# Performance work log

Hardware: AMD Instinct MI355X
Metric: run time of the kernel (lower is better)

Reference implementation:

```python
import jax, jax.numpy as jnp
import numpy as np
from jax import lax

BN_EPS = 1e-3  # Keras BatchNormalization default


def ste_sign(x):
    # larq ste_sign forward: +1 for x >= 0, -1 otherwise
    return jnp.where(x >= 0, 1.0, -1.0).astype(x.dtype)


def conv2d_valid(x, w):
    # x: NHWC, w: HWIO, stride 1, VALID padding
    return lax.conv_general_dilated(
        x, w, window_strides=(1, 1), padding='VALID',
        dimension_numbers=('NHWC', 'HWIO', 'NHWC'))


def maxpool2(x):
    return lax.reduce_window(x, -jnp.inf, lax.max,
                             (1, 2, 2, 1), (1, 2, 2, 1), 'VALID')


def bn_infer(x, mean, var, beta):
    # BatchNormalization(scale=False): center only
    return (x - mean) * lax.rsqrt(var + BN_EPS) + beta


def setup_inputs() -> dict:
    key = jax.random.key(0)
    ks = jax.random.split(key, 16)
    B, H, W, C = 256, 64, 64, 3
    inp = {
        'inputs': jax.random.normal(ks[0], (B, H, W, C), jnp.float32),
        'w1': jax.random.normal(ks[1], (3, 3, 3, 32), jnp.float32) * 0.1,
        'w2': jax.random.normal(ks[2], (3, 3, 32, 64), jnp.float32) * 0.1,
        'w3': jax.random.normal(ks[3], (3, 3, 64, 64), jnp.float32) * 0.1,
        'd1w': jax.random.normal(ks[4], (12 * 12 * 64, 64), jnp.float32) * 0.05,
        'd2w': jax.random.normal(ks[5], (64, 10), jnp.float32) * 0.1,
    }
    for i, (name, c) in enumerate([('bn1', 32), ('bn2', 64), ('bn3', 64), ('bn4', 64), ('bn5', 10)]):
        kk = jax.random.split(ks[6 + i], 3)
        inp[name + '_mean'] = jax.random.normal(kk[0], (c,), jnp.float32) * 0.1
        inp[name + '_var'] = jax.random.uniform(kk[1], (c,), jnp.float32, 0.5, 1.5)
        inp[name + '_beta'] = jax.random.normal(kk[2], (c,), jnp.float32) * 0.1
    return inp


def reference(inputs, w1, w2, w3, d1w, d2w,
              bn1_mean, bn1_var, bn1_beta,
              bn2_mean, bn2_var, bn2_beta,
              bn3_mean, bn3_var, bn3_beta,
              bn4_mean, bn4_var, bn4_beta,
              bn5_mean, bn5_var, bn5_beta):
    # conv1: kernel quantized only (no input quantizer)
    x = conv2d_valid(inputs, ste_sign(w1))           # [B,62,62,32]
    x = maxpool2(x)                                   # [B,31,31,32]
    x = bn_infer(x, bn1_mean, bn1_var, bn1_beta)
    # conv2: input + kernel quantized
    x = conv2d_valid(ste_sign(x), ste_sign(w2))       # [B,29,29,64]
    x = maxpool2(x)                                   # [B,14,14,64]
    x = bn_infer(x, bn2_mean, bn2_var, bn2_beta)
    x = conv2d_valid(ste_sign(x), ste_sign(w3))       # [B,12,12,64]
    x = bn_infer(x, bn3_mean, bn3_var, bn3_beta)
    x = x.reshape(x.shape[0], -1)                     # [B,9216]
    x = ste_sign(x) @ ste_sign(d1w)                   # [B,64]
    x = bn_infer(x, bn4_mean, bn4_var, bn4_beta)
    x = ste_sign(x) @ ste_sign(d2w)                   # [B,10]
    x = bn_infer(x, bn5_mean, bn5_var, bn5_beta)
    return jax.nn.softmax(x, axis=-1)
```

## Files before the change

### kernel.cpp

```cpp
#include <hip/hip_runtime.h>

typedef unsigned int u32;
typedef unsigned long long u64;

#define BN_EPS 1e-3f

static const size_t OFF_BITS1 = 0;
static const size_t OFF_BITS2 = 984064;
static const size_t OFF_BITS3 = 1385472;
static const size_t OFF_BITSD = 1680384;
static const size_t OFF_W2B   = 1682432;
static const size_t OFF_W3B   = 1684736;
static const size_t OFF_D1WB  = 1689344;
static const size_t OFF_D2WB  = 1763072;
static const size_t OFF_T1    = 1763200;
static const size_t OFF_T2    = 1763328;
static const size_t OFF_T3    = 1763584;
static const size_t OFF_T4    = 1763840;

__global__ __launch_bounds__(256) void k_prep(
    const float* __restrict__ w2, const float* __restrict__ w3,
    const float* __restrict__ d1w, const float* __restrict__ d2w,
    const float* __restrict__ m1, const float* __restrict__ v1, const float* __restrict__ be1,
    const float* __restrict__ m2, const float* __restrict__ v2, const float* __restrict__ be2,
    const float* __restrict__ m3, const float* __restrict__ v3, const float* __restrict__ be3,
    const float* __restrict__ m4, const float* __restrict__ v4, const float* __restrict__ be4,
    u32* __restrict__ w2b, u64* __restrict__ w3b, u64* __restrict__ d1wb,
    u64* __restrict__ d2wb, float* __restrict__ t1, float* __restrict__ t2,
    float* __restrict__ t3, float* __restrict__ t4)
{
    int blk = blockIdx.x, tid = threadIdx.x;
    if (blk < 36) {
        int idx = blk * 256 + tid;
        int wi = idx >> 6, oc = idx & 63;
        u64 bits = 0;
        for (int j = 0; j < 64; ++j)
            bits |= (u64)(d1w[(wi * 64 + j) * 64 + oc] >= 0.f) << j;
        d1wb[idx] = bits;
    } else if (blk < 39) {
        int idx = (blk - 36) * 256 + tid;
        if (idx < 576) {
            int tap = idx >> 6, oc = idx & 63;
            u32 bits = 0;
            for (int ic = 0; ic < 32; ++ic)
                bits |= (u32)(w2[(tap * 32 + ic) * 64 + oc] >= 0.f) << ic;
            w2b[idx] = bits;
        }
    } else if (blk < 42) {
        int idx = (blk - 39) * 256 + tid;
        if (idx < 576) {
            int tap = idx >> 6, oc = idx & 63;
            u64 bits = 0;
            for (int ic = 0; ic < 64; ++ic)
                bits |= (u64)(w3[(tap * 64 + ic) * 64 + oc] >= 0.f) << ic;
            w3b[idx] = bits;
        }
    } else {
        if (tid < 32)       t1[tid]      = m1[tid] - be1[tid] * sqrtf(v1[tid] + BN_EPS);
        else if (tid < 96)  { int c = tid - 32;  t2[c] = m2[c] - be2[c] * sqrtf(v2[c] + BN_EPS); }
        else if (tid < 160) { int c = tid - 96;  t3[c] = m3[c] - be3[c] * sqrtf(v3[c] + BN_EPS); }
        else if (tid < 224) { int c = tid - 160; t4[c] = m4[c] - be4[c] * sqrtf(v4[c] + BN_EPS); }
        else if (tid < 234) {
            int oc = tid - 224;
            u64 bits = 0;
            for (int j = 0; j < 64; ++j)
                bits |= (u64)(d2w[j * 10 + oc] >= 0.f) << j;
            d2wb[oc] = bits;
        }
    }
}

__global__ __launch_bounds__(256) void k_conv1(
    const float* __restrict__ inp, const float* __restrict__ w1,
    const float* __restrict__ t1, u32* __restrict__ bits1)
{
    __shared__ float wf[32 * 28];
    __shared__ float t1s[32];
    int tid = threadIdx.x;
    for (int i = tid; i < 864; i += 256) {
        int oc = i / 27, tap = i - oc * 27;
        wf[oc * 28 + tap] = (w1[tap * 32 + oc] >= 0.f) ? 1.f : -1.f;
    }
    if (tid < 32) t1s[tid] = t1[tid];
    __syncthreads();

    int gid = blockIdx.x * 256 + tid;
    int b = gid / 961;
    int p = gid - b * 961;
    int ph = p / 31, pw = p - ph * 31;

    float x[4][4][3];
    const float* base = inp + ((b * 64 + 2 * ph) * 64 + 2 * pw) * 3;
#pragma unroll
    for (int i = 0; i < 4; ++i)
#pragma unroll
        for (int j = 0; j < 4; ++j)
#pragma unroll
            for (int k = 0; k < 3; ++k)
                x[i][j][k] = base[(i * 64 + j) * 3 + k];

    u32 word = 0;
#pragma unroll 1
    for (int oc = 0; oc < 32; ++oc) {
        float wv[28];
        const float4* wq = reinterpret_cast<const float4*>(wf + oc * 28);
#pragma unroll
        for (int q = 0; q < 7; ++q) {
            float4 t = wq[q];
            wv[4 * q] = t.x; wv[4 * q + 1] = t.y; wv[4 * q + 2] = t.z; wv[4 * q + 3] = t.w;
        }
        float s00 = 0.f, s01 = 0.f, s10 = 0.f, s11 = 0.f;
#pragma unroll
        for (int ky = 0; ky < 3; ++ky)
#pragma unroll
            for (int kx = 0; kx < 3; ++kx)
#pragma unroll
                for (int ic = 0; ic < 3; ++ic) {
                    float w = wv[(ky * 3 + kx) * 3 + ic];
                    s00 = fmaf(w, x[ky][kx][ic], s00);
                    s01 = fmaf(w, x[ky][kx + 1][ic], s01);
                    s10 = fmaf(w, x[ky + 1][kx][ic], s10);
                    s11 = fmaf(w, x[ky + 1][kx + 1][ic], s11);
                }
        float m = fmaxf(fmaxf(s00, s01), fmaxf(s10, s11));
        if (m >= t1s[oc]) word |= (1u << oc);
    }
    bits1[gid] = word;
}

__global__ __launch_bounds__(256) void k_conv2(
    const u32* __restrict__ bits1, const u32* __restrict__ w2b,
    const float* __restrict__ t2, u64* __restrict__ bits2)
{
    int lane = threadIdx.x & 63;
    int wid = blockIdx.x * 4 + (threadIdx.x >> 6);
    int b = wid / 196;
    int p = wid - b * 196;
    int ph = p / 14, pw = p - ph * 14;

    const u32* xb = bits1 + b * 961 + (2 * ph) * 31 + 2 * pw;
    u32 xw[4][4];
#pragma unroll
    for (int i = 0; i < 4; ++i)
#pragma unroll
        for (int j = 0; j < 4; ++j)
            xw[i][j] = xb[i * 31 + j];

    u32 wv[9];
#pragma unroll
    for (int t = 0; t < 9; ++t) wv[t] = w2b[t * 64 + lane];

    int mn = 1 << 30;
#pragma unroll
    for (int dy = 0; dy < 2; ++dy)
#pragma unroll
        for (int dx = 0; dx < 2; ++dx) {
            int s = 0;
#pragma unroll
            for (int ky = 0; ky < 3; ++ky)
#pragma unroll
                for (int kx = 0; kx < 3; ++kx)
                    s += __popc(xw[dy + ky][dx + kx] ^ wv[ky * 3 + kx]);
            mn = min(mn, s);
        }
    float val = (float)(288 - 2 * mn);
    u64 word = __ballot(val >= t2[lane]);
    if (lane == 0) bits2[wid] = word;
}

__global__ __launch_bounds__(256) void k_conv3(
    const u64* __restrict__ bits2, const u64* __restrict__ w3b,
    const float* __restrict__ t3, u64* __restrict__ bits3)
{
    int lane = threadIdx.x & 63;
    int wid = blockIdx.x * 4 + (threadIdx.x >> 6);
    int b = wid / 144;
    int p = wid - b * 144;
    int h = p / 12, w = p - h * 12;

    const u64* xb = bits2 + b * 196 + h * 14 + w;
    u64 xw[9];
#pragma unroll
    for (int ky = 0; ky < 3; ++ky)
#pragma unroll
        for (int kx = 0; kx < 3; ++kx)
            xw[ky * 3 + kx] = xb[ky * 14 + kx];

    int s = 0;
#pragma unroll
    for (int t = 0; t < 9; ++t)
        s += __popcll(xw[t] ^ w3b[t * 64 + lane]);
    float val = (float)(576 - 2 * s);
    u64 word = __ballot(val >= t3[lane]);
    if (lane == 0) bits3[wid] = word;
}

__global__ __launch_bounds__(256) void k_dense1(
    const u64* __restrict__ bits3, const u64* __restrict__ d1wb,
    const float* __restrict__ t4, u64* __restrict__ bitsD)
{
    int lane = threadIdx.x & 63;
    int b = blockIdx.x * 4 + (threadIdx.x >> 6);
    const u64* xb = bits3 + b * 144;
    int s = 0;
#pragma unroll 8
    for (int w = 0; w < 144; ++w)
        s += __popcll(xb[w] ^ d1wb[w * 64 + lane]);
    float val = (float)(9216 - 2 * s);
    u64 word = __ballot(val >= t4[lane]);
    if (lane == 0) bitsD[b] = word;
}

__global__ __launch_bounds__(256) void k_dense2(
    const u64* __restrict__ bitsD, const u64* __restrict__ d2wb,
    const float* __restrict__ m5, const float* __restrict__ v5,
    const float* __restrict__ be5, float* __restrict__ out)
{
    int b = threadIdx.x;
    u64 xv = bitsD[b];
    float y[10];
    float mx = -1e30f;
#pragma unroll
    for (int j = 0; j < 10; ++j) {
        int v = 64 - 2 * (int)__popcll(xv ^ d2wb[j]);
        y[j] = ((float)v - m5[j]) * rsqrtf(v5[j] + BN_EPS) + be5[j];
        mx = fmaxf(mx, y[j]);
    }
    float sum = 0.f;
#pragma unroll
    for (int j = 0; j < 10; ++j) { y[j] = expf(y[j] - mx); sum += y[j]; }
    float inv = 1.f / sum;
#pragma unroll
    for (int j = 0; j < 10; ++j) out[b * 10 + j] = y[j] * inv;
}

extern "C" void kernel_launch(void* const* d_in, const int* in_sizes, int n_in,
                              void* d_out, int out_size, void* d_ws, size_t ws_size,
                              hipStream_t stream)
{
    const float* inp = (const float*)d_in[0];
    const float* w1  = (const float*)d_in[1];
    const float* w2  = (const float*)d_in[2];
    const float* w3  = (const float*)d_in[3];
    const float* d1w = (const float*)d_in[4];
    const float* d2w = (const float*)d_in[5];
    const float* m1 = (const float*)d_in[6],  *v1 = (const float*)d_in[7],  *be1 = (const float*)d_in[8];
    const float* m2 = (const float*)d_in[9],  *v2 = (const float*)d_in[10], *be2 = (const float*)d_in[11];
    const float* m3 = (const float*)d_in[12], *v3 = (const float*)d_in[13], *be3 = (const float*)d_in[14];
    const float* m4 = (const float*)d_in[15], *v4 = (const float*)d_in[16], *be4 = (const float*)d_in[17];
    const float* m5 = (const float*)d_in[18], *v5 = (const float*)d_in[19], *be5 = (const float*)d_in[20];

    char* ws = (char*)d_ws;
    u32* bits1 = (u32*)(ws + OFF_BITS1);
    u64* bits2 = (u64*)(ws + OFF_BITS2);
    u64* bits3 = (u64*)(ws + OFF_BITS3);
    u64* bitsD = (u64*)(ws + OFF_BITSD);
    u32* w2b   = (u32*)(ws + OFF_W2B);
    u64* w3b   = (u64*)(ws + OFF_W3B);
    u64* d1wb  = (u64*)(ws + OFF_D1WB);
    u64* d2wb  = (u64*)(ws + OFF_D2WB);
    float* t1  = (float*)(ws + OFF_T1);
    float* t2  = (float*)(ws + OFF_T2);
    float* t3  = (float*)(ws + OFF_T3);
    float* t4  = (float*)(ws + OFF_T4);

    k_prep  <<<43,    256, 0, stream>>>(w2, w3, d1w, d2w,
                                        m1, v1, be1, m2, v2, be2,
                                        m3, v3, be3, m4, v4, be4,
                                        w2b, w3b, d1wb, d2wb, t1, t2, t3, t4);
    k_conv1 <<<961,   256, 0, stream>>>(inp, w1, t1, bits1);
    k_conv2 <<<12544, 256, 0, stream>>>(bits1, w2b, t2, bits2);
    k_conv3 <<<9216,  256, 0, stream>>>(bits2, w3b, t3, bits3);
    k_dense1<<<64,    256, 0, stream>>>(bits3, d1wb, t4, bitsD);
    k_dense2<<<1,     256, 0, stream>>>(bitsD, d2wb, m5, v5, be5, (float*)d_out);
}
```

Baseline: 168.7 us.

## Fuse weight prep into conv1 and conv3+dense1+dense2 into one per-batch kernel

Merges the weight-binarization prep kernel into the conv1 launch as extra blocks, with conv1 computing its own BN threshold inline. Conv3, dense1 and dense2 are fused into one kernel with one block per batch sample. Conv3 output bits stay in shared memory, dense1 is split across four wavefronts with a shared-memory reduction, and softmax uses 16-lane shuffles. This cuts launches from six to three and removes the bits3/bitsD global round trips, but the tail runs only 256 blocks, which may limit parallelism.

```diff
diff --git a/kernel.cpp b/kernel.cpp
--- a/kernel.cpp
+++ b/kernel.cpp
@@ -7,81 +7,78 @@
 
 static const size_t OFF_BITS1 = 0;
 static const size_t OFF_BITS2 = 984064;
-static const size_t OFF_BITS3 = 1385472;
-static const size_t OFF_BITSD = 1680384;
 static const size_t OFF_W2B   = 1682432;
 static const size_t OFF_W3B   = 1684736;
 static const size_t OFF_D1WB  = 1689344;
 static const size_t OFF_D2WB  = 1763072;
-static const size_t OFF_T1    = 1763200;
 static const size_t OFF_T2    = 1763328;
 static const size_t OFF_T3    = 1763584;
 static const size_t OFF_T4    = 1763840;
 
-__global__ __launch_bounds__(256) void k_prep(
+__global__ __launch_bounds__(256) void k_head(
+    const float* __restrict__ inp, const float* __restrict__ w1,
+    const float* __restrict__ m1, const float* __restrict__ v1, const float* __restrict__ be1,
     const float* __restrict__ w2, const float* __restrict__ w3,
     const float* __restrict__ d1w, const float* __restrict__ d2w,
-    const float* __restrict__ m1, const float* __restrict__ v1, const float* __restrict__ be1,
     const float* __restrict__ m2, const float* __restrict__ v2, const float* __restrict__ be2,
     const float* __restrict__ m3, const float* __restrict__ v3, const float* __restrict__ be3,
     const float* __restrict__ m4, const float* __restrict__ v4, const float* __restrict__ be4,
+    u32* __restrict__ bits1,
     u32* __restrict__ w2b, u64* __restrict__ w3b, u64* __restrict__ d1wb,
-    u64* __restrict__ d2wb, float* __restrict__ t1, float* __restrict__ t2,
-    float* __restrict__ t3, float* __restrict__ t4)
-{
-    int blk = blockIdx.x, tid = threadIdx.x;
-    if (blk < 36) {
-        int idx = blk * 256 + tid;
-        int wi = idx >> 6, oc = idx & 63;
-        u64 bits = 0;
-        for (int j = 0; j < 64; ++j)
-            bits |= (u64)(d1w[(wi * 64 + j) * 64 + oc] >= 0.f) << j;
-        d1wb[idx] = bits;
-    } else if (blk < 39) {
-        int idx = (blk - 36) * 256 + tid;
-        if (idx < 576) {
-            int tap = idx >> 6, oc = idx & 63;
-            u32 bits = 0;
-            for (int ic = 0; ic < 32; ++ic)
-                bits |= (u32)(w2[(tap * 32 + ic) * 64 + oc] >= 0.f) << ic;
-            w2b[idx] = bits;
-        }
-    } else if (blk < 42) {
-        int idx = (blk - 39) * 256 + tid;
-        if (idx < 576) {
-            int tap = idx >> 6, oc = idx & 63;
-            u64 bits = 0;
-            for (int ic = 0; ic < 64; ++ic)
-                bits |= (u64)(w3[(tap * 64 + ic) * 64 + oc] >= 0.f) << ic;
-            w3b[idx] = bits;
-        }
-    } else {
-        if (tid < 32)       t1[tid]      = m1[tid] - be1[tid] * sqrtf(v1[tid] + BN_EPS);
-        else if (tid < 96)  { int c = tid - 32;  t2[c] = m2[c] - be2[c] * sqrtf(v2[c] + BN_EPS); }
-        else if (tid < 160) { int c = tid - 96;  t3[c] = m3[c] - be3[c] * sqrtf(v3[c] + BN_EPS); }
-        else if (tid < 224) { int c = tid - 160; t4[c] = m4[c] - be4[c] * sqrtf(v4[c] + BN_EPS); }
-        else if (tid < 234) {
-            int oc = tid - 224;
+    u64* __restrict__ d2wb, float* __restrict__ t2, float* __restrict__ t3,
+    float* __restrict__ t4)
+{
+    int tid = threadIdx.x;
+
+    if (blockIdx.x >= 961) {
+        int pb = blockIdx.x - 961;
+        if (pb < 36) {
+            int idx = pb * 256 + tid;
+            int wi = idx >> 6, oc = idx & 63;
             u64 bits = 0;
             for (int j = 0; j < 64; ++j)
-                bits |= (u64)(d2w[j * 10 + oc] >= 0.f) << j;
-            d2wb[oc] = bits;
-        }
-    }
-}
-
-__global__ __launch_bounds__(256) void k_conv1(
-    const float* __restrict__ inp, const float* __restrict__ w1,
-    const float* __restrict__ t1, u32* __restrict__ bits1)
-{
+                bits |= (u64)(d1w[(wi * 64 + j) * 64 + oc] >= 0.f) << j;
+            d1wb[idx] = bits;
+        } else if (pb < 39) {
+            int idx = (pb - 36) * 256 + tid;
+            if (idx < 576) {
+                int tap = idx >> 6, oc = idx & 63;
+                u32 bits = 0;
+                for (int ic = 0; ic < 32; ++ic)
+                    bits |= (u32)(w2[(tap * 32 + ic) * 64 + oc] >= 0.f) << ic;
+                w2b[idx] = bits;
+            }
+        } else if (pb < 42) {
+            int idx = (pb - 39) * 256 + tid;
+            if (idx < 576) {
+                int tap = idx >> 6, oc = idx & 63;
+                u64 bits = 0;
+                for (int ic = 0; ic < 64; ++ic)
+                    bits |= (u64)(w3[(tap * 64 + ic) * 64 + oc] >= 0.f) << ic;
+                w3b[idx] = bits;
+            }
+        } else {
+            if (tid < 64)        t2[tid] = m2[tid] - be2[tid] * sqrtf(v2[tid] + BN_EPS);
+            else if (tid < 128) { int c = tid - 64;  t3[c] = m3[c] - be3[c] * sqrtf(v3[c] + BN_EPS); }
+            else if (tid < 192) { int c = tid - 128; t4[c] = m4[c] - be4[c] * sqrtf(v4[c] + BN_EPS); }
+            else if (tid < 202) {
+                int oc = tid - 192;
+                u64 bits = 0;
+                for (int j = 0; j < 64; ++j)
+                    bits |= (u64)(d2w[j * 10 + oc] >= 0.f) << j;
+                d2wb[oc] = bits;
+            }
+        }
+        return;
+    }
+
     __shared__ float wf[32 * 28];
     __shared__ float t1s[32];
-    int tid = threadIdx.x;
     for (int i = tid; i < 864; i += 256) {
         int oc = i / 27, tap = i - oc * 27;
         wf[oc * 28 + tap] = (w1[tap * 32 + oc] >= 0.f) ? 1.f : -1.f;
     }
-    if (tid < 32) t1s[tid] = t1[tid];
+    if (tid < 32) t1s[tid] = m1[tid] - be1[tid] * sqrtf(v1[tid] + BN_EPS);
     __syncthreads();
 
     int gid = blockIdx.x * 256 + tid;
@@ -168,70 +165,79 @@
     if (lane == 0) bits2[wid] = word;
 }
 
-__global__ __launch_bounds__(256) void k_conv3(
+__global__ __launch_bounds__(256) void k_tail(
     const u64* __restrict__ bits2, const u64* __restrict__ w3b,
-    const float* __restrict__ t3, u64* __restrict__ bits3)
-{
-    int lane = threadIdx.x & 63;
-    int wid = blockIdx.x * 4 + (threadIdx.x >> 6);
-    int b = wid / 144;
-    int p = wid - b * 144;
-    int h = p / 12, w = p - h * 12;
-
-    const u64* xb = bits2 + b * 196 + h * 14 + w;
-    u64 xw[9];
-#pragma unroll
-    for (int ky = 0; ky < 3; ++ky)
-#pragma unroll
-        for (int kx = 0; kx < 3; ++kx)
-            xw[ky * 3 + kx] = xb[ky * 14 + kx];
-
-    int s = 0;
-#pragma unroll
-    for (int t = 0; t < 9; ++t)
-        s += __popcll(xw[t] ^ w3b[t * 64 + lane]);
-    float val = (float)(576 - 2 * s);
-    u64 word = __ballot(val >= t3[lane]);
-    if (lane == 0) bits3[wid] = word;
-}
-
-__global__ __launch_bounds__(256) void k_dense1(
-    const u64* __restrict__ bits3, const u64* __restrict__ d1wb,
-    const float* __restrict__ t4, u64* __restrict__ bitsD)
-{
-    int lane = threadIdx.x & 63;
-    int b = blockIdx.x * 4 + (threadIdx.x >> 6);
-    const u64* xb = bits3 + b * 144;
-    int s = 0;
-#pragma unroll 8
-    for (int w = 0; w < 144; ++w)
-        s += __popcll(xb[w] ^ d1wb[w * 64 + lane]);
-    float val = (float)(9216 - 2 * s);
-    u64 word = __ballot(val >= t4[lane]);
-    if (lane == 0) bitsD[b] = word;
-}
-
-__global__ __launch_bounds__(256) void k_dense2(
-    const u64* __restrict__ bitsD, const u64* __restrict__ d2wb,
+    const float* __restrict__ t3, const u64* __restrict__ d1wb,
+    const float* __restrict__ t4, const u64* __restrict__ d2wb,
     const float* __restrict__ m5, const float* __restrict__ v5,
     const float* __restrict__ be5, float* __restrict__ out)
 {
-    int b = threadIdx.x;
-    u64 xv = bitsD[b];
-    float y[10];
-    float mx = -1e30f;
-#pragma unroll
-    for (int j = 0; j < 10; ++j) {
-        int v = 64 - 2 * (int)__popcll(xv ^ d2wb[j]);
-        y[j] = ((float)v - m5[j]) * rsqrtf(v5[j] + BN_EPS) + be5[j];
-        mx = fmaxf(mx, y[j]);
-    }
-    float sum = 0.f;
-#pragma unroll
-    for (int j = 0; j < 10; ++j) { y[j] = expf(y[j] - mx); sum += y[j]; }
-    float inv = 1.f / sum;
-#pragma unroll
-    for (int j = 0; j < 10; ++j) out[b * 10 + j] = y[j] * inv;
+    __shared__ u64 sb3[144];
+    __shared__ int part[4][64];
+
+    int tid  = threadIdx.x;
+    int lane = tid & 63;
+    int wv_  = tid >> 6;
+    int b    = blockIdx.x;
+
+    u64 wreg[9];
+#pragma unroll
+    for (int t = 0; t < 9; ++t) wreg[t] = w3b[t * 64 + lane];
+    float t3v = t3[lane];
+
+    const u64* ib = bits2 + b * 196;
+#pragma unroll 2
+    for (int i = 0; i < 36; ++i) {
+        int pos = wv_ * 36 + i;
+        int h = pos / 12, w = pos - h * 12;
+        const u64* xb = ib + h * 14 + w;
+        int s = 0;
+#pragma unroll
+        for (int ky = 0; ky < 3; ++ky)
+#pragma unroll
+            for (int kx = 0; kx < 3; ++kx)
+                s += __popcll(xb[ky * 14 + kx] ^ wreg[ky * 3 + kx]);
+        u64 word = __ballot((float)(576 - 2 * s) >= t3v);
+        if (lane == 0) sb3[pos] = word;
+    }
+    __syncthreads();
+
+    {
+        int q = wv_, oc = lane;
+        int s = 0;
+#pragma unroll 6
+        for (int i = 0; i < 36; ++i) {
+            int w = q * 36 + i;
+            s += __popcll(sb3[w] ^ d1wb[w * 64 + oc]);
+        }
+        part[q][oc] = s;
+    }
+    __syncthreads();
+
+    if (tid < 64) {
+        int s = part[0][tid] + part[1][tid] + part[2][tid] + part[3][tid];
+        float val = (float)(9216 - 2 * s);
+        u64 xv = __ballot(val >= t4[tid]);
+        if (tid < 16) {
+            int j = tid;
+            bool ok = j < 10;
+            float y = -1e30f;
+            if (ok) {
+                int v = 64 - 2 * (int)__popcll(xv ^ d2wb[j]);
+                y = ((float)v - m5[j]) * rsqrtf(v5[j] + BN_EPS) + be5[j];
+            }
+            float mx = y;
+#pragma unroll
+            for (int off = 8; off >= 1; off >>= 1)
+                mx = fmaxf(mx, __shfl_xor(mx, off, 16));
+            float e = ok ? expf(y - mx) : 0.f;
+            float sum = e;
+#pragma unroll
+            for (int off = 8; off >= 1; off >>= 1)
+                sum += __shfl_xor(sum, off, 16);
+            if (ok) out[b * 10 + j] = e / sum;
+        }
+    }
 }
 
 extern "C" void kernel_launch(void* const* d_in, const int* in_sizes, int n_in,
@@ -253,24 +259,19 @@
     char* ws = (char*)d_ws;
     u32* bits1 = (u32*)(ws + OFF_BITS1);
     u64* bits2 = (u64*)(ws + OFF_BITS2);
-    u64* bits3 = (u64*)(ws + OFF_BITS3);
-    u64* bitsD = (u64*)(ws + OFF_BITSD);
     u32* w2b   = (u32*)(ws + OFF_W2B);
     u64* w3b   = (u64*)(ws + OFF_W3B);
     u64* d1wb  = (u64*)(ws + OFF_D1WB);
     u64* d2wb  = (u64*)(ws + OFF_D2WB);
-    float* t1  = (float*)(ws + OFF_T1);
     float* t2  = (float*)(ws + OFF_T2);
     float* t3  = (float*)(ws + OFF_T3);
     float* t4  = (float*)(ws + OFF_T4);
 
-    k_prep  <<<43,    256, 0, stream>>>(w2, w3, d1w, d2w,
-                                        m1, v1, be1, m2, v2, be2,
-                                        m3, v3, be3, m4, v4, be4,
-                                        w2b, w3b, d1wb, d2wb, t1, t2, t3, t4);
-    k_conv1 <<<961,   256, 0, stream>>>(inp, w1, t1, bits1);
-    k_conv2 <<<12544, 256, 0, stream>>>(bits1, w2b, t2, bits2);
-    k_conv3 <<<9216,  256, 0, stream>>>(bits2, w3b, t3, bits3);
-    k_dense1<<<64,    256, 0, stream>>>(bits3, d1wb, t4, bitsD);
-    k_dense2<<<1,     256, 0, stream>>>(bitsD, d2wb, m5, v5, be5, (float*)d_out);
-}
+    k_head <<<1004,  256, 0, stream>>>(inp, w1, m1, v1, be1,
+                                       w2, w3, d1w, d2w,
+                                       m2, v2, be2, m3, v3, be3, m4, v4, be4,
+                                       bits1, w2b, w3b, d1wb, d2wb, t2, t3, t4);
+    k_conv2<<<12544, 256, 0, stream>>>(bits1, w2b, t2, bits2);
+    k_tail <<<256,   256, 0, stream>>>(bits2, w3b, t3, d1wb, t4, d2wb,
+                                       m5, v5, be5, (float*)d_out);
+}
```

After: 146.6 us. 13.1% less time.
